# Optimization experiments

Measured on AMD Instinct MI355X. Metric: run time of the kernel, lower is better.

## Reference

```python
import jax, jax.numpy as jnp
import numpy as np

N_NODES = 100000
N_EDGES = 3200000
IN_DIM = 64
HID_DIM = 128
OUT_DIM = 2


def setup_inputs() -> dict:
    key = jax.random.key(0)
    k1, k2, k3, k4, k5, k6 = jax.random.split(key, 6)
    x = jax.random.normal(k1, (N_NODES, IN_DIM), dtype=jnp.float32)
    edge_index = jax.random.randint(k2, (2, N_EDGES), 0, N_NODES, dtype=jnp.int64)
    W_gcn = jax.random.normal(k3, (IN_DIM, HID_DIM), dtype=jnp.float32) / np.sqrt(IN_DIM)
    b_gcn = jax.random.normal(k4, (HID_DIM,), dtype=jnp.float32) * 0.02
    W_lin = jax.random.normal(k5, (HID_DIM, OUT_DIM), dtype=jnp.float32) / np.sqrt(HID_DIM)
    b_lin = jax.random.normal(k6, (OUT_DIM,), dtype=jnp.float32) * 0.02
    return {"x": x, "edge_index": edge_index, "W_gcn": W_gcn, "b_gcn": b_gcn,
            "W_lin": W_lin, "b_lin": b_lin}


def reference(x, edge_index, W_gcn, b_gcn, W_lin, b_lin):
    # GCNConv (PyG semantics): add self-loops, symmetric deg^{-1/2} norm,
    # aggregate source->target, then relu, dropout(eval=identity), linear.
    N = x.shape[0]
    loop = jnp.arange(N, dtype=edge_index.dtype)
    src = jnp.concatenate([edge_index[0], loop])  # message sources
    dst = jnp.concatenate([edge_index[1], loop])  # message targets

    h = x @ W_gcn  # [N, HID] - transform before propagate (GCNConv order)

    ones = jnp.ones(dst.shape, dtype=h.dtype)
    deg = jax.ops.segment_sum(ones, dst, num_segments=N)  # in-degree incl. self-loop
    dinv = jnp.where(deg > 0, jax.lax.rsqrt(deg), 0.0)
    norm = dinv[src] * dinv[dst]  # [E+N]

    msg = h[src] * norm[:, None]                      # irregular gather
    agg = jax.ops.segment_sum(msg, dst, num_segments=N)  # irregular scatter-add
    agg = agg + b_gcn

    # relu -> dropout(p=0.5, eval mode => identity) -> linear head
    return jax.nn.relu(agg) @ W_lin + b_lin  # [N, OUT_DIM]
```

## Files before the change

kernel.cpp:

```cpp
#include <hip/hip_runtime.h>
#include <hip/hip_fp16.h>

#define N_NODES 100000
#define N_EDGES 3200000
#define IN_DIM 64
#define HID_DIM 128

#define RNODES 128
#define NRANGE 782
#define PCHUNK 512
#define PCHSZ (N_EDGES / PCHUNK)
#define TCAP 28
#define NLCAP 4608


__global__ __launch_bounds__(256) void part_kernel(const int* __restrict__ src,
                                                   const int* __restrict__ dst,
                                                   int* __restrict__ tmp,
                                                   int* __restrict__ tcnt) {
    __shared__ int cur[NRANGE];
    const int c = blockIdx.x, tid = threadIdx.x;
    for (int i = tid; i < NRANGE; i += 256) cur[i] = 0;
    __syncthreads();
    const int e0 = c * PCHSZ;
    const int2* s2 = (const int2*)(src + e0);
    const int2* d2 = (const int2*)(dst + e0);
    for (int i = tid; i < PCHSZ / 2; i += 256) {
        const int2 dd = d2[i];
        const int2 ss = s2[i];
        {
            const int r = dd.x >> 7;
            const int pos = atomicAdd(&cur[r], 1);
            if (pos < TCAP) tmp[(size_t)(r * PCHUNK + c) * TCAP + pos] = ss.x | ((dd.x & 127) << 17);
        }
        {
            const int r = dd.y >> 7;
            const int pos = atomicAdd(&cur[r], 1);
            if (pos < TCAP) tmp[(size_t)(r * PCHUNK + c) * TCAP + pos] = ss.y | ((dd.y & 127) << 17);
        }
    }
    __syncthreads();
    for (int i = tid; i < NRANGE; i += 256)
        tcnt[i * PCHUNK + c] = min(cur[i], TCAP);
}

__global__ __launch_bounds__(512) void degscale_kernel(const int* __restrict__ tmp,
                                                       const int* __restrict__ tcnt,
                                                       const float* __restrict__ x,
                                                       int* __restrict__ degn,
                                                       float* __restrict__ dinv,
                                                       __half* __restrict__ y) {
    __shared__ int   cnt[RNODES];
    __shared__ float dvs[RNODES];
    const int r = blockIdx.x, tid = threadIdx.x;
    if (tid < RNODES) cnt[tid] = 0;
    __syncthreads();
    {
        const int n = tcnt[r * PCHUNK + tid];
        const int* t = tmp + (size_t)(r * PCHUNK + tid) * TCAP;
        for (int i = 0; i < n; ++i) atomicAdd(&cnt[t[i] >> 17], 1);
    }
    __syncthreads();
    if (tid < RNODES) {
        const int node = r * RNODES + tid;
        const int dg = cnt[tid];
        degn[node] = dg;
        const float dv = rsqrtf((float)dg + 1.0f);
        dvs[tid] = dv;
        if (node < N_NODES) dinv[node] = dv;
    }
    __syncthreads();
    for (int i = tid; i < RNODES * 16; i += 512) {
        const int nl = i >> 4, q = i & 15;
        const int node = r * RNODES + nl;
        if (node < N_NODES) {
            const float4 v = ((const float4*)x)[(size_t)node * 16 + q];
            const float dv = dvs[nl];
            __half2 h0 = __floats2half2_rn(v.x * dv, v.y * dv);
            __half2 h1 = __floats2half2_rn(v.z * dv, v.w * dv);
            uint2 pk;
            pk.x = *(unsigned int*)&h0;
            pk.y = *(unsigned int*)&h1;
            ((uint2*)y)[(size_t)node * 16 + q] = pk;
        }
    }
}

__global__ __launch_bounds__(512) void aggb_kernel(const int* __restrict__ tmp,
                                                   const int* __restrict__ tcnt,
                                                   const int* __restrict__ degn,
                                                   const __half* __restrict__ y,
                                                   __half* __restrict__ agg) {
    __shared__ int nodelist[NLCAP];
    __shared__ int sc[RNODES];
    __shared__ int start[RNODES];
    __shared__ int cur[RNODES];
    const int r = blockIdx.x, tid = threadIdx.x;

    int mydeg = 0;
    if (tid < RNODES) {
        mydeg = degn[r * RNODES + tid];
        sc[tid] = mydeg;
    }
    __syncthreads();
    #pragma unroll
    for (int off = 1; off < RNODES; off <<= 1) {
        int v = 0;
        if (tid < RNODES && tid >= off) v = sc[tid - off];
        __syncthreads();
        if (tid < RNODES) sc[tid] += v;
        __syncthreads();
    }
    if (tid < RNODES) {
        start[tid] = sc[tid] - mydeg;
        cur[tid]   = sc[tid] - mydeg;
    }
    __syncthreads();

    {
        const int n = tcnt[r * PCHUNK + tid];
        const int* t = tmp + (size_t)(r * PCHUNK + tid) * TCAP;
        for (int i = 0; i < n; ++i) {
            const int pk = t[i];
            const int slot = atomicAdd(&cur[pk >> 17], 1);
            if (slot < NLCAP) nodelist[slot] = pk & 0x1FFFF;
        }
    }
    __syncthreads();

    const int g = tid >> 3, lane = tid & 7;
    const uint4* y16 = (const uint4*)y;
    for (int nl = g; nl < RNODES; nl += 64) {
        const int node = r * RNODES + nl;
        if (node >= N_NODES) continue;
        float accf[8];
        {
            const uint4 pk = y16[(size_t)node * 8 + lane];
            const __half2* h = (const __half2*)&pk;
            #pragma unroll
            for (int q = 0; q < 4; ++q) {
                const float2 f = __half22float2(h[q]);
                accf[2*q] = f.x; accf[2*q+1] = f.y;
            }
        }
        const int beg = start[nl], end = sc[nl];
        int j = beg;
        for (; j + 4 <= end; j += 4) {
            const int s0 = nodelist[j];
            const int s1 = nodelist[j + 1];
            const int s2 = nodelist[j + 2];
            const int s3 = nodelist[j + 3];
            const uint4 p0 = y16[(size_t)s0 * 8 + lane];
            const uint4 p1 = y16[(size_t)s1 * 8 + lane];
            const uint4 p2 = y16[(size_t)s2 * 8 + lane];
            const uint4 p3 = y16[(size_t)s3 * 8 + lane];
            const __half2* h0 = (const __half2*)&p0;
            const __half2* h1 = (const __half2*)&p1;
            const __half2* h2 = (const __half2*)&p2;
            const __half2* h3 = (const __half2*)&p3;
            #pragma unroll
            for (int q = 0; q < 4; ++q) {
                float2 f0 = __half22float2(h0[q]);
                float2 f1 = __half22float2(h1[q]);
                float2 f2 = __half22float2(h2[q]);
                float2 f3 = __half22float2(h3[q]);
                accf[2*q]   += (f0.x + f1.x) + (f2.x + f3.x);
                accf[2*q+1] += (f0.y + f1.y) + (f2.y + f3.y);
            }
        }
        for (; j < end; ++j) {
            const int s = nodelist[j];
            const uint4 pk = y16[(size_t)s * 8 + lane];
            const __half2* h = (const __half2*)&pk;
            #pragma unroll
            for (int q = 0; q < 4; ++q) {
                const float2 f = __half22float2(h[q]);
                accf[2*q] += f.x; accf[2*q+1] += f.y;
            }
        }
        uint4 o;
        __half2* oh = (__half2*)&o;
        #pragma unroll
        for (int q = 0; q < 4; ++q)
            oh[q] = __floats2half2_rn(accf[2*q], accf[2*q+1]);
        ((uint4*)agg)[(size_t)node * 8 + lane] = o;
    }
}

#define H_NPB 32
__global__ __launch_bounds__(256) void head_kernel(const __half* __restrict__ agg,
                                                   const float* __restrict__ dinv,
                                                   const float* __restrict__ W,
                                                   const float* __restrict__ b_gcn,
                                                   const float* __restrict__ W_lin,
                                                   const float* __restrict__ b_lin,
                                                   float* __restrict__ out) {
    __shared__ float4 Ws[IN_DIM * HID_DIM / 4];
    __shared__ float  as[H_NPB * IN_DIM];
    const int tid = threadIdx.x;

    const float4* W4 = (const float4*)W;
    #pragma unroll
    for (int i = tid; i < IN_DIM * HID_DIM / 4; i += 256) Ws[i] = W4[i];

    const int node0 = blockIdx.x * H_NPB;
    {
        const uint4 a4 = ((const uint4*)(agg + (size_t)node0 * IN_DIM))[tid];
        const __half2* h = (const __half2*)&a4;
        #pragma unroll
        for (int q = 0; q < 4; ++q) {
            const float2 f = __half22float2(h[q]);
            as[tid * 8 + 2*q]     = f.x;
            as[tid * 8 + 2*q + 1] = f.y;
        }
    }
    __syncthreads();

    const int jq = tid & 31;
    const int ng = tid >> 5;
    const float* arow = as + ng * 4 * IN_DIM;

    float4 a0 = {0,0,0,0}, a1 = {0,0,0,0}, a2 = {0,0,0,0}, a3 = {0,0,0,0};
    for (int k = 0; k < IN_DIM; ++k) {
        const float4 wv = Ws[k * 32 + jq];
        const float v0 = arow[k];
        const float v1 = arow[IN_DIM + k];
        const float v2 = arow[2 * IN_DIM + k];
        const float v3 = arow[3 * IN_DIM + k];
        a0.x += v0*wv.x; a0.y += v0*wv.y; a0.z += v0*wv.z; a0.w += v0*wv.w;
        a1.x += v1*wv.x; a1.y += v1*wv.y; a1.z += v1*wv.z; a1.w += v1*wv.w;
        a2.x += v2*wv.x; a2.y += v2*wv.y; a2.z += v2*wv.z; a2.w += v2*wv.w;
        a3.x += v3*wv.x; a3.y += v3*wv.y; a3.z += v3*wv.z; a3.w += v3*wv.w;
    }

    const float4 bg = ((const float4*)b_gcn)[jq];
    const int c0 = jq * 4;
    const float w00 = W_lin[(c0+0)*2], w01 = W_lin[(c0+0)*2+1];
    const float w10 = W_lin[(c0+1)*2], w11 = W_lin[(c0+1)*2+1];
    const float w20 = W_lin[(c0+2)*2], w21 = W_lin[(c0+2)*2+1];
    const float w30 = W_lin[(c0+3)*2], w31 = W_lin[(c0+3)*2+1];
    const float bl0 = b_lin[0], bl1 = b_lin[1];

    float4 am[4] = {a0, a1, a2, a3};
    #pragma unroll
    for (int m = 0; m < 4; ++m) {
        const int node = node0 + ng * 4 + m;
        const float dv = dinv[node];
        float4 v;
        v.x = fmaxf(am[m].x * dv + bg.x, 0.f);
        v.y = fmaxf(am[m].y * dv + bg.y, 0.f);
        v.z = fmaxf(am[m].z * dv + bg.z, 0.f);
        v.w = fmaxf(am[m].w * dv + bg.w, 0.f);
        float o0 = v.x*w00 + v.y*w10 + v.z*w20 + v.w*w30;
        float o1 = v.x*w01 + v.y*w11 + v.z*w21 + v.w*w31;
        #pragma unroll
        for (int off = 16; off > 0; off >>= 1) {
            o0 += __shfl_down(o0, off, 32);
            o1 += __shfl_down(o1, off, 32);
        }
        if (jq == 0) {
            out[(size_t)node * 2 + 0] = o0 + bl0;
            out[(size_t)node * 2 + 1] = o1 + bl1;
        }
    }
}

extern "C" void kernel_launch(void* const* d_in, const int* in_sizes, int n_in,
                              void* d_out, int out_size, void* d_ws, size_t ws_size,
                              hipStream_t stream) {
    const float* x     = (const float*)d_in[0];
    const int*   ei    = (const int*)  d_in[1];
    const float* W_gcn = (const float*)d_in[2];
    const float* b_gcn = (const float*)d_in[3];
    const float* W_lin = (const float*)d_in[4];
    const float* b_lin = (const float*)d_in[5];
    float* out = (float*)d_out;

    int*    tmp  = (int*)d_ws;
    int*    tcnt = tmp + (size_t)NRANGE * PCHUNK * TCAP;
    int*    degn = tcnt + NRANGE * PCHUNK;
    float*  dinv = (float*)(degn + NRANGE * RNODES);
    __half* y    = (__half*)(dinv + N_NODES);
    __half* agg  = y + (size_t)N_NODES * IN_DIM;

    const int* src = ei;
    const int* dst = ei + N_EDGES;

    part_kernel<<<PCHUNK, 256, 0, stream>>>(src, dst, tmp, tcnt);
    degscale_kernel<<<NRANGE, 512, 0, stream>>>(tmp, tcnt, x, degn, dinv, y);
    aggb_kernel<<<NRANGE, 512, 0, stream>>>(tmp, tcnt, degn, y, agg);
    head_kernel<<<N_NODES / H_NPB, 256, 0, stream>>>(agg, dinv, W_gcn, b_gcn, W_lin, b_lin, out);
}
```

Baseline: 243.5 us.

## Split each destination range across two half-blocks in degree and aggregation kernels

The degree/scale and aggregation kernels now launch two blocks per 128-node destination range. Each block handles 64 nodes and filters the range's partitioned edges by the top bit of the local destination index. This doubles the grid and shrinks per-block shared memory, aiming for better occupancy and more parallelism. The cost is that every block reads the full tmp bucket for its range, so bucket reads double. The partition kernel also moves to 512 threads per block.

Result: slower. 289.0 us (+18.7%).

```diff
diff --git a/kernel.cpp b/kernel.cpp
--- a/kernel.cpp
+++ b/kernel.cpp
@@ -8,24 +8,26 @@
 
 #define RNODES 128
 #define NRANGE 782
+#define HRNODES 64
+#define NHALF 1564
 #define PCHUNK 512
 #define PCHSZ (N_EDGES / PCHUNK)
 #define TCAP 28
-#define NLCAP 4608
-
-
-__global__ __launch_bounds__(256) void part_kernel(const int* __restrict__ src,
+#define NLCAP 2432
+
+
+__global__ __launch_bounds__(512) void part_kernel(const int* __restrict__ src,
                                                    const int* __restrict__ dst,
                                                    int* __restrict__ tmp,
                                                    int* __restrict__ tcnt) {
     __shared__ int cur[NRANGE];
     const int c = blockIdx.x, tid = threadIdx.x;
-    for (int i = tid; i < NRANGE; i += 256) cur[i] = 0;
+    for (int i = tid; i < NRANGE; i += 512) cur[i] = 0;
     __syncthreads();
     const int e0 = c * PCHSZ;
     const int2* s2 = (const int2*)(src + e0);
     const int2* d2 = (const int2*)(dst + e0);
-    for (int i = tid; i < PCHSZ / 2; i += 256) {
+    for (int i = tid; i < PCHSZ / 2; i += 512) {
         const int2 dd = d2[i];
         const int2 ss = s2[i];
         {
@@ -40,29 +42,33 @@
         }
     }
     __syncthreads();
-    for (int i = tid; i < NRANGE; i += 256)
+    for (int i = tid; i < NRANGE; i += 512)
         tcnt[i * PCHUNK + c] = min(cur[i], TCAP);
 }
 
-__global__ __launch_bounds__(512) void degscale_kernel(const int* __restrict__ tmp,
+__global__ __launch_bounds__(256) void degscale_kernel(const int* __restrict__ tmp,
                                                        const int* __restrict__ tcnt,
                                                        const float* __restrict__ x,
                                                        int* __restrict__ degn,
                                                        float* __restrict__ dinv,
                                                        __half* __restrict__ y) {
-    __shared__ int   cnt[RNODES];
-    __shared__ float dvs[RNODES];
-    const int r = blockIdx.x, tid = threadIdx.x;
-    if (tid < RNODES) cnt[tid] = 0;
-    __syncthreads();
-    {
-        const int n = tcnt[r * PCHUNK + tid];
-        const int* t = tmp + (size_t)(r * PCHUNK + tid) * TCAP;
-        for (int i = 0; i < n; ++i) atomicAdd(&cnt[t[i] >> 17], 1);
-    }
-    __syncthreads();
-    if (tid < RNODES) {
-        const int node = r * RNODES + tid;
+    __shared__ int   cnt[HRNODES];
+    __shared__ float dvs[HRNODES];
+    const int r2 = blockIdx.x, tid = threadIdx.x;
+    const int r = r2 >> 1, half = r2 & 1;
+    if (tid < HRNODES) cnt[tid] = 0;
+    __syncthreads();
+    for (int t = tid; t < PCHUNK; t += 256) {
+        const int n = tcnt[r * PCHUNK + t];
+        const int* tp = tmp + (size_t)(r * PCHUNK + t) * TCAP;
+        for (int i = 0; i < n; ++i) {
+            const int dloc = tp[i] >> 17;
+            if ((dloc >> 6) == half) atomicAdd(&cnt[dloc & 63], 1);
+        }
+    }
+    __syncthreads();
+    if (tid < HRNODES) {
+        const int node = r2 * HRNODES + tid;
         const int dg = cnt[tid];
         degn[node] = dg;
         const float dv = rsqrtf((float)dg + 1.0f);
@@ -70,9 +76,9 @@
         if (node < N_NODES) dinv[node] = dv;
     }
     __syncthreads();
-    for (int i = tid; i < RNODES * 16; i += 512) {
+    for (int i = tid; i < HRNODES * 16; i += 256) {
         const int nl = i >> 4, q = i & 15;
-        const int node = r * RNODES + nl;
+        const int node = r2 * HRNODES + nl;
         if (node < N_NODES) {
             const float4 v = ((const float4*)x)[(size_t)node * 16 + q];
             const float dv = dvs[nl];
@@ -86,52 +92,56 @@
     }
 }
 
-__global__ __launch_bounds__(512) void aggb_kernel(const int* __restrict__ tmp,
+__global__ __launch_bounds__(256) void aggb_kernel(const int* __restrict__ tmp,
                                                    const int* __restrict__ tcnt,
                                                    const int* __restrict__ degn,
                                                    const __half* __restrict__ y,
                                                    __half* __restrict__ agg) {
     __shared__ int nodelist[NLCAP];
-    __shared__ int sc[RNODES];
-    __shared__ int start[RNODES];
-    __shared__ int cur[RNODES];
-    const int r = blockIdx.x, tid = threadIdx.x;
+    __shared__ int sc[HRNODES];
+    __shared__ int start[HRNODES];
+    __shared__ int cur[HRNODES];
+    const int r2 = blockIdx.x, tid = threadIdx.x;
+    const int r = r2 >> 1, half = r2 & 1;
 
     int mydeg = 0;
-    if (tid < RNODES) {
-        mydeg = degn[r * RNODES + tid];
+    if (tid < HRNODES) {
+        mydeg = degn[r2 * HRNODES + tid];
         sc[tid] = mydeg;
     }
     __syncthreads();
     #pragma unroll
-    for (int off = 1; off < RNODES; off <<= 1) {
+    for (int off = 1; off < HRNODES; off <<= 1) {
         int v = 0;
-        if (tid < RNODES && tid >= off) v = sc[tid - off];
+        if (tid < HRNODES && tid >= off) v = sc[tid - off];
         __syncthreads();
-        if (tid < RNODES) sc[tid] += v;
+        if (tid < HRNODES) sc[tid] += v;
         __syncthreads();
     }
-    if (tid < RNODES) {
+    if (tid < HRNODES) {
         start[tid] = sc[tid] - mydeg;
         cur[tid]   = sc[tid] - mydeg;
     }
     __syncthreads();
 
-    {
-        const int n = tcnt[r * PCHUNK + tid];
-        const int* t = tmp + (size_t)(r * PCHUNK + tid) * TCAP;
+    for (int t = tid; t < PCHUNK; t += 256) {
+        const int n = tcnt[r * PCHUNK + t];
+        const int* tp = tmp + (size_t)(r * PCHUNK + t) * TCAP;
         for (int i = 0; i < n; ++i) {
-            const int pk = t[i];
-            const int slot = atomicAdd(&cur[pk >> 17], 1);
-            if (slot < NLCAP) nodelist[slot] = pk & 0x1FFFF;
+            const int pk = tp[i];
+            const int dloc = pk >> 17;
+            if ((dloc >> 6) == half) {
+                const int slot = atomicAdd(&cur[dloc & 63], 1);
+                if (slot < NLCAP) nodelist[slot] = pk & 0x1FFFF;
+            }
         }
     }
     __syncthreads();
 
     const int g = tid >> 3, lane = tid & 7;
     const uint4* y16 = (const uint4*)y;
-    for (int nl = g; nl < RNODES; nl += 64) {
-        const int node = r * RNODES + nl;
+    for (int nl = g; nl < HRNODES; nl += 32) {
+        const int node = r2 * HRNODES + nl;
         if (node >= N_NODES) continue;
         float accf[8];
         {
@@ -279,15 +289,15 @@
     int*    tmp  = (int*)d_ws;
     int*    tcnt = tmp + (size_t)NRANGE * PCHUNK * TCAP;
     int*    degn = tcnt + NRANGE * PCHUNK;
-    float*  dinv = (float*)(degn + NRANGE * RNODES);
+    float*  dinv = (float*)(degn + NHALF * HRNODES);
     __half* y    = (__half*)(dinv + N_NODES);
     __half* agg  = y + (size_t)N_NODES * IN_DIM;
 
     const int* src = ei;
     const int* dst = ei + N_EDGES;
 
-    part_kernel<<<PCHUNK, 256, 0, stream>>>(src, dst, tmp, tcnt);
-    degscale_kernel<<<NRANGE, 512, 0, stream>>>(tmp, tcnt, x, degn, dinv, y);
-    aggb_kernel<<<NRANGE, 512, 0, stream>>>(tmp, tcnt, degn, y, agg);
+    part_kernel<<<PCHUNK, 512, 0, stream>>>(src, dst, tmp, tcnt);
+    degscale_kernel<<<NHALF, 256, 0, stream>>>(tmp, tcnt, x, degn, dinv, y);
+    aggb_kernel<<<NHALF, 256, 0, stream>>>(tmp, tcnt, degn, y, agg);
     head_kernel<<<N_NODES / H_NPB, 256, 0, stream>>>(agg, dinv, W_gcn, b_gcn, W_lin, b_lin, out);
 }
```

## Split fp16 features into lo/hi halves and gather in two passes

Applied to the files above, without the earlier changes.

The scaled fp16 feature table and the aggregate are stored as two separate 32-column halves. The aggregation kernel runs two passes, one per half, so each pass gathers from a 6.4MB table, which improves cache hit rates on the random neighbour reads. It also maps 4 lanes per node instead of 8, so all 128 nodes in a block are handled at once rather than looping. The partition kernel moves to 512 threads. The cost is that the nodelist and indices are read twice, and there is per-node load imbalance across lanes.

New measurement: 262.8 us. +8.0%, slower.

```diff
diff --git a/kernel.cpp b/kernel.cpp
--- a/kernel.cpp
+++ b/kernel.cpp
@@ -14,18 +14,18 @@
 #define NLCAP 4608
 
 
-__global__ __launch_bounds__(256) void part_kernel(const int* __restrict__ src,
+__global__ __launch_bounds__(512) void part_kernel(const int* __restrict__ src,
                                                    const int* __restrict__ dst,
                                                    int* __restrict__ tmp,
                                                    int* __restrict__ tcnt) {
     __shared__ int cur[NRANGE];
     const int c = blockIdx.x, tid = threadIdx.x;
-    for (int i = tid; i < NRANGE; i += 256) cur[i] = 0;
+    for (int i = tid; i < NRANGE; i += 512) cur[i] = 0;
     __syncthreads();
     const int e0 = c * PCHSZ;
     const int2* s2 = (const int2*)(src + e0);
     const int2* d2 = (const int2*)(dst + e0);
-    for (int i = tid; i < PCHSZ / 2; i += 256) {
+    for (int i = tid; i < PCHSZ / 2; i += 512) {
         const int2 dd = d2[i];
         const int2 ss = s2[i];
         {
@@ -40,7 +40,7 @@
         }
     }
     __syncthreads();
-    for (int i = tid; i < NRANGE; i += 256)
+    for (int i = tid; i < NRANGE; i += 512)
         tcnt[i * PCHUNK + c] = min(cur[i], TCAP);
 }
 
@@ -49,7 +49,8 @@
                                                        const float* __restrict__ x,
                                                        int* __restrict__ degn,
                                                        float* __restrict__ dinv,
-                                                       __half* __restrict__ y) {
+                                                       __half* __restrict__ y_lo,
+                                                       __half* __restrict__ y_hi) {
     __shared__ int   cnt[RNODES];
     __shared__ float dvs[RNODES];
     const int r = blockIdx.x, tid = threadIdx.x;
@@ -57,8 +58,8 @@
     __syncthreads();
     {
         const int n = tcnt[r * PCHUNK + tid];
-        const int* t = tmp + (size_t)(r * PCHUNK + tid) * TCAP;
-        for (int i = 0; i < n; ++i) atomicAdd(&cnt[t[i] >> 17], 1);
+        const int* tp = tmp + (size_t)(r * PCHUNK + tid) * TCAP;
+        for (int i = 0; i < n; ++i) atomicAdd(&cnt[tp[i] >> 17], 1);
     }
     __syncthreads();
     if (tid < RNODES) {
@@ -81,7 +82,8 @@
             uint2 pk;
             pk.x = *(unsigned int*)&h0;
             pk.y = *(unsigned int*)&h1;
-            ((uint2*)y)[(size_t)node * 16 + q] = pk;
+            if (q < 8) ((uint2*)y_lo)[(size_t)node * 8 + q]       = pk;
+            else       ((uint2*)y_hi)[(size_t)node * 8 + (q - 8)] = pk;
         }
     }
 }
@@ -89,8 +91,10 @@
 __global__ __launch_bounds__(512) void aggb_kernel(const int* __restrict__ tmp,
                                                    const int* __restrict__ tcnt,
                                                    const int* __restrict__ degn,
-                                                   const __half* __restrict__ y,
-                                                   __half* __restrict__ agg) {
+                                                   const __half* __restrict__ y_lo,
+                                                   const __half* __restrict__ y_hi,
+                                                   __half* __restrict__ agg_lo,
+                                                   __half* __restrict__ agg_hi) {
     __shared__ int nodelist[NLCAP];
     __shared__ int sc[RNODES];
     __shared__ int start[RNODES];
@@ -119,76 +123,82 @@
 
     {
         const int n = tcnt[r * PCHUNK + tid];
-        const int* t = tmp + (size_t)(r * PCHUNK + tid) * TCAP;
+        const int* tp = tmp + (size_t)(r * PCHUNK + tid) * TCAP;
         for (int i = 0; i < n; ++i) {
-            const int pk = t[i];
+            const int pk = tp[i];
             const int slot = atomicAdd(&cur[pk >> 17], 1);
             if (slot < NLCAP) nodelist[slot] = pk & 0x1FFFF;
         }
     }
     __syncthreads();
 
-    const int g = tid >> 3, lane = tid & 7;
-    const uint4* y16 = (const uint4*)y;
-    for (int nl = g; nl < RNODES; nl += 64) {
-        const int node = r * RNODES + nl;
-        if (node >= N_NODES) continue;
+    const int g = tid >> 2, lane = tid & 3;
+    const int node = r * RNODES + g;
+    const bool live = (node < N_NODES);
+    const int beg = start[g], end = sc[g];
+
+    const uint4* ylo4 = (const uint4*)y_lo;
+    const uint4* yhi4 = (const uint4*)y_hi;
+
+    for (int pass = 0; pass < 2; ++pass) {
+        const uint4* yp = pass ? yhi4 : ylo4;
         float accf[8];
-        {
-            const uint4 pk = y16[(size_t)node * 8 + lane];
+        if (live) {
+            const uint4 pk = yp[(size_t)node * 4 + lane];
             const __half2* h = (const __half2*)&pk;
             #pragma unroll
             for (int q = 0; q < 4; ++q) {
                 const float2 f = __half22float2(h[q]);
                 accf[2*q] = f.x; accf[2*q+1] = f.y;
             }
-        }
-        const int beg = start[nl], end = sc[nl];
-        int j = beg;
-        for (; j + 4 <= end; j += 4) {
-            const int s0 = nodelist[j];
-            const int s1 = nodelist[j + 1];
-            const int s2 = nodelist[j + 2];
-            const int s3 = nodelist[j + 3];
-            const uint4 p0 = y16[(size_t)s0 * 8 + lane];
-            const uint4 p1 = y16[(size_t)s1 * 8 + lane];
-            const uint4 p2 = y16[(size_t)s2 * 8 + lane];
-            const uint4 p3 = y16[(size_t)s3 * 8 + lane];
-            const __half2* h0 = (const __half2*)&p0;
-            const __half2* h1 = (const __half2*)&p1;
-            const __half2* h2 = (const __half2*)&p2;
-            const __half2* h3 = (const __half2*)&p3;
+            int j = beg;
+            for (; j + 4 <= end; j += 4) {
+                const int s0 = nodelist[j];
+                const int s1 = nodelist[j + 1];
+                const int s2 = nodelist[j + 2];
+                const int s3 = nodelist[j + 3];
+                const uint4 p0 = yp[(size_t)s0 * 4 + lane];
+                const uint4 p1 = yp[(size_t)s1 * 4 + lane];
+                const uint4 p2 = yp[(size_t)s2 * 4 + lane];
+                const uint4 p3 = yp[(size_t)s3 * 4 + lane];
+                const __half2* h0 = (const __half2*)&p0;
+                const __half2* h1 = (const __half2*)&p1;
+                const __half2* h2 = (const __half2*)&p2;
+                const __half2* h3 = (const __half2*)&p3;
+                #pragma unroll
+                for (int q = 0; q < 4; ++q) {
+                    float2 f0 = __half22float2(h0[q]);
+                    float2 f1 = __half22float2(h1[q]);
+                    float2 f2 = __half22float2(h2[q]);
+                    float2 f3 = __half22float2(h3[q]);
+                    accf[2*q]   += (f0.x + f1.x) + (f2.x + f3.x);
+                    accf[2*q+1] += (f0.y + f1.y) + (f2.y + f3.y);
+                }
+            }
+            for (; j < end; ++j) {
+                const int s = nodelist[j];
+                const uint4 pk2 = yp[(size_t)s * 4 + lane];
+                const __half2* h2p = (const __half2*)&pk2;
+                #pragma unroll
+                for (int q = 0; q < 4; ++q) {
+                    const float2 f = __half22float2(h2p[q]);
+                    accf[2*q] += f.x; accf[2*q+1] += f.y;
+                }
+            }
+            uint4 o;
+            __half2* oh = (__half2*)&o;
             #pragma unroll
-            for (int q = 0; q < 4; ++q) {
-                float2 f0 = __half22float2(h0[q]);
-                float2 f1 = __half22float2(h1[q]);
-                float2 f2 = __half22float2(h2[q]);
-                float2 f3 = __half22float2(h3[q]);
-                accf[2*q]   += (f0.x + f1.x) + (f2.x + f3.x);
-                accf[2*q+1] += (f0.y + f1.y) + (f2.y + f3.y);
-            }
-        }
-        for (; j < end; ++j) {
-            const int s = nodelist[j];
-            const uint4 pk = y16[(size_t)s * 8 + lane];
-            const __half2* h = (const __half2*)&pk;
-            #pragma unroll
-            for (int q = 0; q < 4; ++q) {
-                const float2 f = __half22float2(h[q]);
-                accf[2*q] += f.x; accf[2*q+1] += f.y;
-            }
-        }
-        uint4 o;
-        __half2* oh = (__half2*)&o;
-        #pragma unroll
-        for (int q = 0; q < 4; ++q)
-            oh[q] = __floats2half2_rn(accf[2*q], accf[2*q+1]);
-        ((uint4*)agg)[(size_t)node * 8 + lane] = o;
+            for (int q = 0; q < 4; ++q)
+                oh[q] = __floats2half2_rn(accf[2*q], accf[2*q+1]);
+            if (pass) ((uint4*)agg_hi)[(size_t)node * 4 + lane] = o;
+            else      ((uint4*)agg_lo)[(size_t)node * 4 + lane] = o;
+        }
     }
 }
 
 #define H_NPB 32
-__global__ __launch_bounds__(256) void head_kernel(const __half* __restrict__ agg,
+__global__ __launch_bounds__(256) void head_kernel(const __half* __restrict__ agg_lo,
+                                                   const __half* __restrict__ agg_hi,
                                                    const float* __restrict__ dinv,
                                                    const float* __restrict__ W,
                                                    const float* __restrict__ b_gcn,
@@ -205,13 +215,18 @@
 
     const int node0 = blockIdx.x * H_NPB;
     {
-        const uint4 a4 = ((const uint4*)(agg + (size_t)node0 * IN_DIM))[tid];
+        const int t = tid & 127;
+        const int nl = t >> 2, part = t & 3;
+        const uint4 a4 = (tid < 128)
+            ? ((const uint4*)agg_lo)[(size_t)(node0 + nl) * 4 + part]
+            : ((const uint4*)agg_hi)[(size_t)(node0 + nl) * 4 + part];
         const __half2* h = (const __half2*)&a4;
+        float* dstp = as + nl * IN_DIM + ((tid < 128) ? 0 : 32) + part * 8;
         #pragma unroll
         for (int q = 0; q < 4; ++q) {
             const float2 f = __half22float2(h[q]);
-            as[tid * 8 + 2*q]     = f.x;
-            as[tid * 8 + 2*q + 1] = f.y;
+            dstp[2*q]     = f.x;
+            dstp[2*q + 1] = f.y;
         }
     }
     __syncthreads();
@@ -276,18 +291,21 @@
     const float* b_lin = (const float*)d_in[5];
     float* out = (float*)d_out;
 
-    int*    tmp  = (int*)d_ws;
-    int*    tcnt = tmp + (size_t)NRANGE * PCHUNK * TCAP;
-    int*    degn = tcnt + NRANGE * PCHUNK;
-    float*  dinv = (float*)(degn + NRANGE * RNODES);
-    __half* y    = (__half*)(dinv + N_NODES);
-    __half* agg  = y + (size_t)N_NODES * IN_DIM;
+    int*    tmp    = (int*)d_ws;
+    int*    tcnt   = tmp + (size_t)NRANGE * PCHUNK * TCAP;
+    int*    degn   = tcnt + NRANGE * PCHUNK;
+    float*  dinv   = (float*)(degn + NRANGE * RNODES);
+    __half* y_lo   = (__half*)(dinv + N_NODES);
+    __half* y_hi   = y_lo + (size_t)N_NODES * 32;
+    __half* agg_lo = y_hi + (size_t)N_NODES * 32;
+    __half* agg_hi = agg_lo + (size_t)N_NODES * 32;
 
     const int* src = ei;
     const int* dst = ei + N_EDGES;
 
-    part_kernel<<<PCHUNK, 256, 0, stream>>>(src, dst, tmp, tcnt);
-    degscale_kernel<<<NRANGE, 512, 0, stream>>>(tmp, tcnt, x, degn, dinv, y);
-    aggb_kernel<<<NRANGE, 512, 0, stream>>>(tmp, tcnt, degn, y, agg);
-    head_kernel<<<N_NODES / H_NPB, 256, 0, stream>>>(agg, dinv, W_gcn, b_gcn, W_lin, b_lin, out);
-}
+    part_kernel<<<PCHUNK, 512, 0, stream>>>(src, dst, tmp, tcnt);
+    degscale_kernel<<<NRANGE, 512, 0, stream>>>(tmp, tcnt, x, degn, dinv, y_lo, y_hi);
+    aggb_kernel<<<NRANGE, 512, 0, stream>>>(tmp, tcnt, degn, y_lo, y_hi, agg_lo, agg_hi);
+    head_kernel<<<N_NODES / H_NPB, 256, 0, stream>>>(agg_lo, agg_hi, dinv,
+                                                     W_gcn, b_gcn, W_lin, b_lin, out);
+}
```
